# Optimization experiments

Measured on AMD Instinct MI355X. Metric: run time of the kernel, lower is better.

Reference implementation:

```python
import jax, jax.numpy as jnp
import numpy as np

B, S, H, A, C = 2, 128, 1024, 256, 14


def setup_inputs() -> dict:
    key = jax.random.key(0)
    ks = jax.random.split(key, 20)
    def p(k, shape, scale=0.02):
        return jax.random.normal(k, shape, dtype=jnp.float32) * scale
    inp = {"memory": jax.random.normal(ks[0], (B, S, H), dtype=jnp.float32)}
    i = 1
    for name in ("h", "t", "m"):
        inp[f"{name}_W1"] = p(ks[i], (H, A)); i += 1
        inp[f"{name}_b1"] = jnp.zeros((A,), jnp.float32)
        inp[f"{name}_W2"] = p(ks[i], (A, A)); i += 1
        inp[f"{name}_b2"] = jnp.zeros((A,), jnp.float32)
        inp[f"s0{name}_W"] = p(ks[i], (A, C)); i += 1
        inp[f"s0{name}_b"] = jnp.zeros((C,), jnp.float32)
        inp[f"s1{name}_W"] = p(ks[i], (A, C)); i += 1
        inp[f"s1{name}_b"] = jnp.zeros((C,), jnp.float32)
    inp["uni"] = jax.random.normal(ks[i], (C,), dtype=jnp.float32)
    return inp


def _mlp(x, W1, b1, W2, b2):
    # 2-layer MLP (Linear -> ReLU -> Linear), dropout=0 / eval mode
    return jax.nn.relu(x @ W1 + b1) @ W2 + b2


def reference(memory,
              h_W1, h_b1, h_W2, h_b2, s0h_W, s0h_b, s1h_W, s1h_b,
              t_W1, t_b1, t_W2, t_b2, s0t_W, s0t_b, s1t_W, s1t_b,
              m_W1, m_b1, m_W2, m_b2, s0m_W, s0m_b, s1m_W, s1m_b,
              uni):
    seq = memory.shape[1]
    head = _mlp(memory, h_W1, h_b1, h_W2, h_b2)   # [B,S,A]
    tail = _mlp(memory, t_W1, t_b1, t_W2, t_b2)
    mid = _mlp(memory, m_W1, m_b1, m_W2, m_b2)

    sh0 = head @ s0h_W + s0h_b   # [B,S,C]
    st0 = tail @ s0t_W + s0t_b
    sm0 = mid @ s0m_W + s0m_b
    # score[b,i,j,k,c] = sh0[b,i,c] + st0[b,j,c] + sm0[b,k,c]
    score = sh0[:, :, None, None, :] + st0[:, None, :, None, :] + sm0[:, None, None, :, :]

    idx = jnp.arange(seq)
    # mask where k > j or k < i (mid index must lie in [head, tail])
    bad = (idx[None, None, :] > idx[None, :, None]) | (idx[None, None, :] < idx[:, None, None])  # [S,S,S]
    score = jnp.where(bad[None, :, :, :, None], jnp.float32(-1e6), score)

    alpha = jax.nn.softmax(score, axis=3)  # softmax over mid index k

    sh1 = head @ s1h_W + s1h_b  # note: original uses head/tail/mid (not head1) for score1
    st1 = tail @ s1t_W + s1t_b
    sm1 = mid @ s1m_W + s1m_b
    score1 = sh1[:, :, None, None, :] + st1[:, None, :, None, :] + sm1[:, None, None, :, :]

    final_score = jnp.sum(alpha * score1, axis=3) + uni[None, None, None, :]  # [B,S,S,C]
    return final_score
```

## Files before the change

### kernel.cpp

```cpp
#include <hip/hip_runtime.h>

#define BB 2
#define SS 128
#define HH 1024
#define AA 256
#define CC 14
#define R_TOT (BB*SS)

struct NetP { const float *W1,*b1,*W2,*b2,*s0W,*s0b,*s1W,*s1b; };
struct AllP { NetP n[3]; };

#define S0_OFF 0
#define S1_OFF (3*R_TOT*CC)
#define P_OFF  (2*3*R_TOT*CC)
#define Q_OFF  (P_OFF + BB*(SS+1)*CC)
#define MEAN_OFF (Q_OFF + BB*(SS+1)*CC)

__global__ __launch_bounds__(512)
void hid_kernel(const float* __restrict__ mem, AllP P, float* __restrict__ hid)
{
    const int bx  = blockIdx.x;
    const int net = bx >> 7;
    const int rem = bx & 127;
    const int rt  = rem >> 2;
    const int ct  = rem & 3;
    const int row0 = rt * 8;
    const int lane = threadIdx.x & 63;
    const int wv   = __builtin_amdgcn_readfirstlane(threadIdx.x >> 6);
    const int col  = ct*64 + lane;
    const NetP p = P.n[net];

    __shared__ float part[8][8][64];

    float acc[8] = {0,0,0,0,0,0,0,0};
    const int k0 = wv * 128;
    const float* __restrict__ W1p  = p.W1 + (size_t)k0*AA + col;
    const float* __restrict__ memp = mem + (size_t)(net*0 + row0)*HH + k0;
    #pragma unroll 8
    for (int kk = 0; kk < 128; ++kk) {
        const float w = W1p[(size_t)kk*AA];
        #pragma unroll
        for (int r = 0; r < 8; ++r)
            acc[r] = fmaf(memp[(size_t)r*HH + kk], w, acc[r]);
    }
    #pragma unroll
    for (int r = 0; r < 8; ++r) part[wv][r][lane] = acc[r];
    __syncthreads();

    const int r = threadIdx.x >> 6;
    const int l = threadIdx.x & 63;
    float s = p.b1[ct*64 + l];
    #pragma unroll
    for (int w = 0; w < 8; ++w) s += part[w][r][l];
    hid[((size_t)net*R_TOT + row0 + r)*AA + ct*64 + l] = fmaxf(s, 0.f);
}

__global__ __launch_bounds__(512)
void out_kernel(const float* __restrict__ hid, AllP P,
                float* __restrict__ s0o, float* __restrict__ s1o)
{
    const int bx  = blockIdx.x;
    const int net = bx >> 6;
    const int rt  = bx & 63;
    const int row0 = rt * 4;
    const NetP p = P.n[net];
    const int col = threadIdx.x & 255;
    const int kh  = __builtin_amdgcn_readfirstlane(threadIdx.x >> 8);

    __shared__ float part[2][4][256];
    __shared__ float outp[4][256];
    __shared__ float pp[112][4];

    const float* __restrict__ hb = hid + ((size_t)net*R_TOT + row0)*AA;
    float acc[4] = {0,0,0,0};
    const int k0 = kh * 128;
    const float* __restrict__ W2p = p.W2 + (size_t)k0*AA + col;
    #pragma unroll 8
    for (int kk = 0; kk < 128; ++kk) {
        const float w = W2p[(size_t)kk*AA];
        #pragma unroll
        for (int r = 0; r < 4; ++r)
            acc[r] = fmaf(hb[(size_t)r*AA + k0 + kk], w, acc[r]);
    }
    #pragma unroll
    for (int r = 0; r < 4; ++r) part[kh][r][col] = acc[r];
    __syncthreads();

    for (int i = threadIdx.x; i < 4*AA; i += 512) {
        const int r = i >> 8, u = i & 255;
        outp[r][u] = part[0][r][u] + part[1][r][u] + p.b2[u];
    }
    __syncthreads();

    const int t = threadIdx.x;
    if (t < 448) {
        const int task = t >> 2, kc = t & 3;
        const int which = (task >= 56) ? 1 : 0;
        const int rem2  = task - which*56;
        const int rr = rem2 / CC, c = rem2 % CC;
        const float* __restrict__ W = which ? p.s1W : p.s0W;
        float s = 0.f;
        #pragma unroll 4
        for (int k = kc*64; k < kc*64 + 64; ++k)
            s = fmaf(outp[rr][k], W[(size_t)k*CC + c], s);
        pp[task][kc] = s;
    }
    __syncthreads();
    if (t < 112) {
        const int which = (t >= 56) ? 1 : 0;
        const int rem2  = t - which*56;
        const int rr = rem2 / CC, c = rem2 % CC;
        const float s = pp[t][0]+pp[t][1]+pp[t][2]+pp[t][3] + (which ? p.s1b : p.s0b)[c];
        (which ? s1o : s0o)[((size_t)net*R_TOT + row0 + rr)*CC + c] = s;
    }
}

__global__ __launch_bounds__(128)
void prefix_kernel(const float* __restrict__ s0w, const float* __restrict__ s1w,
                   float* __restrict__ Pp, float* __restrict__ Qp,
                   float* __restrict__ meanp)
{
    const int b = blockIdx.x / CC, c = blockIdx.x % CC;
    const int k = threadIdx.x;
    const int lane = k & 63, wv = k >> 6;
    const float x0 = s0w[(size_t)(2*R_TOT + b*SS + k)*CC + c];
    const float x1 = s1w[(size_t)(2*R_TOT + b*SS + k)*CC + c];
    __shared__ float smx[2], se[2], sq[2], ssm[2];

    float m = x0;
    #pragma unroll
    for (int off = 32; off >= 1; off >>= 1) m = fmaxf(m, __shfl_xor(m, off));
    float s1sum = x1;
    #pragma unroll
    for (int off = 32; off >= 1; off >>= 1) s1sum += __shfl_xor(s1sum, off);
    if (lane == 0) { smx[wv] = m; ssm[wv] = s1sum; }
    __syncthreads();
    const float M = fmaxf(smx[0], smx[1]);

    float e = __expf(x0 - M);
    float q = e * x1;
    #pragma unroll
    for (int off = 1; off <= 32; off <<= 1) {
        const float te = __shfl_up(e, off);
        const float tq = __shfl_up(q, off);
        if (lane >= off) { e += te; q += tq; }
    }
    if (lane == 63) { se[wv] = e; sq[wv] = q; }
    __syncthreads();
    if (wv == 1) { e += se[0]; q += sq[0]; }

    const size_t base = ((size_t)b*(SS+1))*CC + c;
    Pp[base + (size_t)(k+1)*CC] = e;
    Qp[base + (size_t)(k+1)*CC] = q;
    if (k == 0) {
        Pp[base] = 0.f;
        Qp[base] = 0.f;
        meanp[b*CC + c] = (ssm[0] + ssm[1]) * (1.f/SS);
    }
}

__global__ __launch_bounds__(512)
void final_kernel(const float* __restrict__ s1w,
                  const float* __restrict__ Pp, const float* __restrict__ Qp,
                  const float* __restrict__ meanp, const float* __restrict__ uni,
                  float* __restrict__ out)
{
    const int bi = blockIdx.x;
    const int b = bi >> 7, i = bi & (SS-1);
    __shared__ float sh1L[CC], uniL[CC], mnL[CC], PiL[CC], QiL[CC];
    if (threadIdx.x < CC) {
        const int c = threadIdx.x;
        sh1L[c] = s1w[(size_t)bi*CC + c];
        uniL[c] = uni[c];
        mnL[c]  = meanp[b*CC + c];
        PiL[c]  = Pp[((size_t)b*(SS+1) + i)*CC + c];
        QiL[c]  = Qp[((size_t)b*(SS+1) + i)*CC + c];
    }
    __syncthreads();
    const float* __restrict__ st1 = s1w + (size_t)(R_TOT + b*SS)*CC;
    const float* __restrict__ Pj  = Pp + ((size_t)b*(SS+1) + 1)*CC;
    const float* __restrict__ Qj  = Qp + ((size_t)b*(SS+1) + 1)*CC;
    float* __restrict__ o = out + (size_t)bi*SS*CC;
    for (int idx = threadIdx.x; idx < SS*CC; idx += 512) {
        const int j = idx / CC, c = idx - j*CC;
        float add;
        if (i <= j) add = (Qj[idx] - QiL[c]) / (Pj[idx] - PiL[c]);
        else        add = mnL[c];
        o[idx] = sh1L[c] + st1[idx] + uniL[c] + add;
    }
}

extern "C" void kernel_launch(void* const* d_in, const int* in_sizes, int n_in,
                              void* d_out, int out_size, void* d_ws, size_t ws_size,
                              hipStream_t stream)
{
    const float* mem = (const float*)d_in[0];
    AllP P;
    for (int n = 0; n < 3; ++n) {
        const int base = 1 + 8*n;
        P.n[n].W1  = (const float*)d_in[base+0];
        P.n[n].b1  = (const float*)d_in[base+1];
        P.n[n].W2  = (const float*)d_in[base+2];
        P.n[n].b2  = (const float*)d_in[base+3];
        P.n[n].s0W = (const float*)d_in[base+4];
        P.n[n].s0b = (const float*)d_in[base+5];
        P.n[n].s1W = (const float*)d_in[base+6];
        P.n[n].s1b = (const float*)d_in[base+7];
    }
    const float* uni = (const float*)d_in[25];
    float* ws = (float*)d_ws;
    float* s0 = ws + S0_OFF;
    float* s1 = ws + S1_OFF;
    float* Pp = ws + P_OFF;
    float* Qp = ws + Q_OFF;
    float* mn = ws + MEAN_OFF;
    float* out = (float*)d_out;
    float* hid = out;

    hipLaunchKernelGGL(hid_kernel,    dim3(384),   dim3(512), 0, stream, mem, P, hid);
    hipLaunchKernelGGL(out_kernel,    dim3(192),   dim3(512), 0, stream, hid, P, s0, s1);
    hipLaunchKernelGGL(prefix_kernel, dim3(BB*CC), dim3(128), 0, stream, s0, s1, Pp, Qp, mn);
    hipLaunchKernelGGL(final_kernel,  dim3(BB*SS), dim3(512), 0, stream, s1, Pp, Qp, mn, uni, out);
}
```

Before: 33.34 us.

## Fuse prefix softmax scan into final kernel and vectorize output stores

Removes the separate prefix kernel: each final-kernel block recomputes the per-batch prefix sums of exp(sm0) and exp(sm0)*sm1 into shared memory, then reads them from LDS instead of global memory. This drops one kernel launch and a global round trip, at the cost of redundant scan work in every block (256 blocks each scan 14 columns). Output is written with float4 stores, and the hidden buffer moves from the output array to the workspace.

```diff
diff --git a/kernel.cpp b/kernel.cpp
--- a/kernel.cpp
+++ b/kernel.cpp
@@ -12,9 +12,7 @@
 
 #define S0_OFF 0
 #define S1_OFF (3*R_TOT*CC)
-#define P_OFF  (2*3*R_TOT*CC)
-#define Q_OFF  (P_OFF + BB*(SS+1)*CC)
-#define MEAN_OFF (Q_OFF + BB*(SS+1)*CC)
+#define HID_OFF 32768
 
 __global__ __launch_bounds__(512)
 void hid_kernel(const float* __restrict__ mem, AllP P, float* __restrict__ hid)
@@ -35,7 +33,7 @@
     float acc[8] = {0,0,0,0,0,0,0,0};
     const int k0 = wv * 128;
     const float* __restrict__ W1p  = p.W1 + (size_t)k0*AA + col;
-    const float* __restrict__ memp = mem + (size_t)(net*0 + row0)*HH + k0;
+    const float* __restrict__ memp = mem + (size_t)row0*HH + k0;
     #pragma unroll 8
     for (int kk = 0; kk < 128; ++kk) {
         const float w = W1p[(size_t)kk*AA];
@@ -115,78 +113,88 @@
     }
 }
 
-__global__ __launch_bounds__(128)
-void prefix_kernel(const float* __restrict__ s0w, const float* __restrict__ s1w,
-                   float* __restrict__ Pp, float* __restrict__ Qp,
-                   float* __restrict__ meanp)
-{
-    const int b = blockIdx.x / CC, c = blockIdx.x % CC;
-    const int k = threadIdx.x;
-    const int lane = k & 63, wv = k >> 6;
-    const float x0 = s0w[(size_t)(2*R_TOT + b*SS + k)*CC + c];
-    const float x1 = s1w[(size_t)(2*R_TOT + b*SS + k)*CC + c];
-    __shared__ float smx[2], se[2], sq[2], ssm[2];
-
-    float m = x0;
-    #pragma unroll
-    for (int off = 32; off >= 1; off >>= 1) m = fmaxf(m, __shfl_xor(m, off));
-    float s1sum = x1;
-    #pragma unroll
-    for (int off = 32; off >= 1; off >>= 1) s1sum += __shfl_xor(s1sum, off);
-    if (lane == 0) { smx[wv] = m; ssm[wv] = s1sum; }
-    __syncthreads();
-    const float M = fmaxf(smx[0], smx[1]);
-
-    float e = __expf(x0 - M);
-    float q = e * x1;
-    #pragma unroll
-    for (int off = 1; off <= 32; off <<= 1) {
-        const float te = __shfl_up(e, off);
-        const float tq = __shfl_up(q, off);
-        if (lane >= off) { e += te; q += tq; }
-    }
-    if (lane == 63) { se[wv] = e; sq[wv] = q; }
-    __syncthreads();
-    if (wv == 1) { e += se[0]; q += sq[0]; }
-
-    const size_t base = ((size_t)b*(SS+1))*CC + c;
-    Pp[base + (size_t)(k+1)*CC] = e;
-    Qp[base + (size_t)(k+1)*CC] = q;
-    if (k == 0) {
-        Pp[base] = 0.f;
-        Qp[base] = 0.f;
-        meanp[b*CC + c] = (ssm[0] + ssm[1]) * (1.f/SS);
-    }
-}
-
 __global__ __launch_bounds__(512)
-void final_kernel(const float* __restrict__ s1w,
-                  const float* __restrict__ Pp, const float* __restrict__ Qp,
-                  const float* __restrict__ meanp, const float* __restrict__ uni,
-                  float* __restrict__ out)
+void final_kernel(const float* __restrict__ s0w, const float* __restrict__ s1w,
+                  const float* __restrict__ uni, float* __restrict__ out)
 {
     const int bi = blockIdx.x;
     const int b = bi >> 7, i = bi & (SS-1);
-    __shared__ float sh1L[CC], uniL[CC], mnL[CC], PiL[CC], QiL[CC];
-    if (threadIdx.x < CC) {
-        const int c = threadIdx.x;
-        sh1L[c] = s1w[(size_t)bi*CC + c];
-        uniL[c] = uni[c];
-        mnL[c]  = meanp[b*CC + c];
-        PiL[c]  = Pp[((size_t)b*(SS+1) + i)*CC + c];
-        QiL[c]  = Qp[((size_t)b*(SS+1) + i)*CC + c];
-    }
-    __syncthreads();
+    const int tid = threadIdx.x;
+    const int lane = tid & 63;
+    const int k    = tid & 127;
+    const int wv2  = (tid >> 6) & 1;
+    const int slot = tid >> 7;
+
+    __shared__ float E[SS*CC];
+    __shared__ float Qe[SS*CC];
+    __shared__ float red[4][4][2];
+    __shared__ float mnL[CC], sh1L[CC], uniL[CC];
+
+    if (tid < CC) {
+        sh1L[tid] = s1w[(size_t)bi*CC + tid];
+        uniL[tid] = uni[tid];
+    }
+
+    const float* __restrict__ sm0b = s0w + (size_t)(2*R_TOT + b*SS)*CC;
+    const float* __restrict__ sm1b = s1w + (size_t)(2*R_TOT + b*SS)*CC;
+
+    for (int pass = 0; pass < 4; ++pass) {
+        const int c = pass*4 + slot;
+        float x0 = 0.f, x1 = 0.f, e = 0.f, q = 0.f;
+        if (c < CC) {
+            x0 = sm0b[(size_t)k*CC + c];
+            x1 = sm1b[(size_t)k*CC + c];
+            float m = x0;
+            #pragma unroll
+            for (int off = 32; off >= 1; off >>= 1) m = fmaxf(m, __shfl_xor(m, off));
+            float ss = x1;
+            #pragma unroll
+            for (int off = 32; off >= 1; off >>= 1) ss += __shfl_xor(ss, off);
+            if (lane == 0) { red[0][slot][wv2] = m; red[1][slot][wv2] = ss; }
+        }
+        __syncthreads();
+        if (c < CC) {
+            const float M = fmaxf(red[0][slot][0], red[0][slot][1]);
+            e = __expf(x0 - M);
+            q = e * x1;
+            #pragma unroll
+            for (int off = 1; off <= 32; off <<= 1) {
+                const float te = __shfl_up(e, off);
+                const float tq = __shfl_up(q, off);
+                if (lane >= off) { e += te; q += tq; }
+            }
+            if (lane == 63) { red[2][slot][wv2] = e; red[3][slot][wv2] = q; }
+        }
+        __syncthreads();
+        if (c < CC) {
+            if (wv2 == 1) { e += red[2][slot][0]; q += red[3][slot][0]; }
+            E [k*CC + c] = e;
+            Qe[k*CC + c] = q;
+            if (k == 0) mnL[c] = (red[1][slot][0] + red[1][slot][1]) * (1.f/SS);
+        }
+        __syncthreads();
+    }
+
     const float* __restrict__ st1 = s1w + (size_t)(R_TOT + b*SS)*CC;
-    const float* __restrict__ Pj  = Pp + ((size_t)b*(SS+1) + 1)*CC;
-    const float* __restrict__ Qj  = Qp + ((size_t)b*(SS+1) + 1)*CC;
     float* __restrict__ o = out + (size_t)bi*SS*CC;
-    for (int idx = threadIdx.x; idx < SS*CC; idx += 512) {
-        const int j = idx / CC, c = idx - j*CC;
-        float add;
-        if (i <= j) add = (Qj[idx] - QiL[c]) / (Pj[idx] - PiL[c]);
-        else        add = mnL[c];
-        o[idx] = sh1L[c] + st1[idx] + uniL[c] + add;
+    if (tid < 448) {
+        const int e0 = tid * 4;
+        float v[4];
+        #pragma unroll
+        for (int u = 0; u < 4; ++u) {
+            const int idx = e0 + u;
+            const int j = idx / CC, c = idx - j*CC;
+            float add;
+            if (i <= j) {
+                const float Ei = (i > 0) ? E [(i-1)*CC + c] : 0.f;
+                const float Qi = (i > 0) ? Qe[(i-1)*CC + c] : 0.f;
+                add = (Qe[j*CC + c] - Qi) / (E[j*CC + c] - Ei);
+            } else {
+                add = mnL[c];
+            }
+            v[u] = sh1L[c] + st1[idx] + uniL[c] + add;
+        }
+        *(float4*)&o[e0] = make_float4(v[0], v[1], v[2], v[3]);
     }
 }
 
@@ -208,17 +216,13 @@
         P.n[n].s1b = (const float*)d_in[base+7];
     }
     const float* uni = (const float*)d_in[25];
-    float* ws = (float*)d_ws;
-    float* s0 = ws + S0_OFF;
-    float* s1 = ws + S1_OFF;
-    float* Pp = ws + P_OFF;
-    float* Qp = ws + Q_OFF;
-    float* mn = ws + MEAN_OFF;
+    float* ws  = (float*)d_ws;
+    float* s0  = ws + S0_OFF;
+    float* s1  = ws + S1_OFF;
+    float* hid = ws + HID_OFF;
     float* out = (float*)d_out;
-    float* hid = out;
-
-    hipLaunchKernelGGL(hid_kernel,    dim3(384),   dim3(512), 0, stream, mem, P, hid);
-    hipLaunchKernelGGL(out_kernel,    dim3(192),   dim3(512), 0, stream, hid, P, s0, s1);
-    hipLaunchKernelGGL(prefix_kernel, dim3(BB*CC), dim3(128), 0, stream, s0, s1, Pp, Qp, mn);
-    hipLaunchKernelGGL(final_kernel,  dim3(BB*SS), dim3(512), 0, stream, s1, Pp, Qp, mn, uni, out);
-}
+
+    hipLaunchKernelGGL(hid_kernel,   dim3(384),    dim3(512), 0, stream, mem, P, hid);
+    hipLaunchKernelGGL(out_kernel,   dim3(192),    dim3(512), 0, stream, hid, P, s0, s1);
+    hipLaunchKernelGGL(final_kernel, dim3(BB*SS),  dim3(512), 0, stream, s0, s1, uni, out);
+}
```

Result: no change. 33.16 us (-0.5%).
